# Optimization experiments

Hardware: AMD Instinct MI355X
Metric: run time of the kernel (lower is better)

Reference implementation:

```python
import jax, jax.numpy as jnp
import numpy as np

DIM = 512
DEPTH = 4
HEADS = 8
MLP = 4096
HEAD_DIM = DIM // HEADS
SCALE = HEAD_DIM ** -0.5
EPS = 1e-5


def setup_inputs() -> dict:
    key = jax.random.key(0)
    ks = jax.random.split(key, 14)
    B, C, H, W, D = 1, DIM, 16, 16, 16
    x = jax.random.normal(ks[0], (B, C, H, W, D), dtype=jnp.float32)
    s = 0.02
    inp = {
        'x': x,
        # GroupNorm(1, C) affine params per layer
        'g1': jnp.ones((DEPTH, C), jnp.float32),
        'b1': jnp.zeros((DEPTH, C), jnp.float32),
        'g2': jnp.ones((DEPTH, C), jnp.float32),
        'b2': jnp.zeros((DEPTH, C), jnp.float32),
        # 1x1 conv weights act as channel matmuls
        'wq': jax.random.normal(ks[1], (DEPTH, C, C), jnp.float32) * s,
        'wk': jax.random.normal(ks[2], (DEPTH, C, C), jnp.float32) * s,
        'wv': jax.random.normal(ks[3], (DEPTH, C, C), jnp.float32) * s,
        'wp': jax.random.normal(ks[4], (DEPTH, C, C), jnp.float32) * s,
        'bp': jnp.zeros((DEPTH, C), jnp.float32),
        'w1': jax.random.normal(ks[5], (DEPTH, MLP, C), jnp.float32) * s,
        'bb1': jnp.zeros((DEPTH, MLP), jnp.float32),
        'w2': jax.random.normal(ks[6], (DEPTH, C, MLP), jnp.float32) * s,
        'bb2': jnp.zeros((DEPTH, C), jnp.float32),
    }
    return inp


def _groupnorm1(x, g, b):
    # GroupNorm(num_groups=1): normalize over (C,H,W,D) per sample, per-channel affine
    mu = jnp.mean(x, axis=(1, 2, 3, 4), keepdims=True)
    var = jnp.mean(jnp.square(x - mu), axis=(1, 2, 3, 4), keepdims=True)
    xn = (x - mu) * jax.lax.rsqrt(var + EPS)
    return xn * g[None, :, None, None, None] + b[None, :, None, None, None]


def _attention(x, wq, wk, wv, wp, bp):
    B, C, H, W, D = x.shape
    N = H * W * D
    xf = x.reshape(B, C, N)
    # 1x1 conv == channel matmul; then the module's non-standard view:
    # C split as (head_dim, num_heads)
    q = jnp.einsum('oc,bcn->bon', wq, xf).reshape(B, HEAD_DIM, HEADS, N)
    k = jnp.einsum('oc,bcn->bon', wk, xf).reshape(B, HEAD_DIM, HEADS, N)
    v = jnp.einsum('oc,bcn->bon', wv, xf).reshape(B, HEAD_DIM, HEADS, N)
    attn = jnp.einsum('bchn,bchm->bhnm', q, k) * SCALE  # [B,H,N,N]
    attn = jax.nn.softmax(attn, axis=-1)
    o = jnp.einsum('bhnm,bchm->bchn', attn, v).reshape(B, C, N)
    o = jnp.einsum('oc,bcn->bon', wp, o) + bp[None, :, None]
    return o.reshape(B, C, H, W, D)


def _feedforward(x, w1, bb1, w2, bb2):
    B, C, H, W, D = x.shape
    N = H * W * D
    xf = x.reshape(B, C, N)
    h = jax.nn.relu(jnp.einsum('mc,bcn->bmn', w1, xf) + bb1[None, :, None])
    o = jnp.einsum('cm,bmn->bcn', w2, h) + bb2[None, :, None]
    return o.reshape(B, C, H, W, D)


def reference(x, g1, b1, g2, b2, wq, wk, wv, wp, bp, w1, bb1, w2, bb2):
    for l in range(DEPTH):
        x = x + _attention(_groupnorm1(x, g1[l], b1[l]), wq[l], wk[l], wv[l], wp[l], bp[l])
        x = x + _feedforward(_groupnorm1(x, g2[l], b2[l]), w1[l], bb1[l], w2[l], bb2[l])
    return x
```

## Files before the change

kernel.cpp:

```cpp
#include <hip/hip_runtime.h>

#define CDIM   512
#define NTOK   4096
#define TOT    (CDIM*NTOK)
#define MLPD   4096
#define EPS    1e-5f
#define QSCALE 0.1803368801111204f

typedef _Float16 f16;
typedef _Float16 f16x4 __attribute__((ext_vector_type(4)));
typedef _Float16 f16x8 __attribute__((ext_vector_type(8)));
typedef float    f32x4 __attribute__((ext_vector_type(4)));

typedef __attribute__((address_space(3))) void lds_void;
typedef const __attribute__((address_space(1))) void glb_void;

__device__ __forceinline__ void gload16(const void* g, void* l) {
  __builtin_amdgcn_global_load_lds((glb_void*)g, (lds_void*)l, 16, 0, 0);
}

__device__ __forceinline__ f32x4 zero4() { f32x4 z; z[0]=0.f; z[1]=0.f; z[2]=0.f; z[3]=0.f; return z; }

__global__ __launch_bounds__(256) void cvt_qkv(const float* __restrict__ wq,
                                               const float* __restrict__ wk,
                                               const float* __restrict__ wv,
                                               f16* __restrict__ dst) {
  int i = blockIdx.x * 256 + threadIdx.x;
  int k0 = (i & 63) * 8;
  int rowglob = i >> 6;
  int l = rowglob / 1536;
  int n = rowglob - l * 1536;
  int sect = n >> 9, nn = n & 511;
  int h = nn >> 6, hd = nn & 63;
  int c = hd * 8 + h;
  const float* base = (sect == 0) ? wq : (sect == 1) ? wk : wv;
  const float* src = base + (size_t)l * 262144 + c * 512 + k0;
  float scl = (sect == 0) ? QSCALE : 1.f;
  float4 a = *(const float4*)src;
  float4 b = *(const float4*)(src + 4);
  f16x8 o;
  o[0]=(f16)(a.x*scl); o[1]=(f16)(a.y*scl); o[2]=(f16)(a.z*scl); o[3]=(f16)(a.w*scl);
  o[4]=(f16)(b.x*scl); o[5]=(f16)(b.y*scl); o[6]=(f16)(b.z*scl); o[7]=(f16)(b.w*scl);
  *(f16x8*)&dst[(size_t)l * 786432 + (size_t)n * 512 + k0] = o;
}

__global__ __launch_bounds__(256) void cvt_wp(const float* __restrict__ wp,
                                              f16* __restrict__ dst) {
  int i = blockIdx.x * 256 + threadIdx.x;
  int d0 = (i & 63) * 8;
  int rowglob = i >> 6;
  int l = rowglob >> 9, n = rowglob & 511;
  int h = d0 >> 6;
  const float* src = wp + (size_t)l * 262144 + (size_t)n * 512;
  f16x8 o;
#pragma unroll
  for (int u = 0; u < 8; ++u) {
    int hd = (d0 + u) & 63;
    o[u] = (f16)src[hd * 8 + h];
  }
  *(f16x8*)&dst[(size_t)l * 262144 + (size_t)n * 512 + d0] = o;
}

__global__ __launch_bounds__(256) void cvt_12(const float* __restrict__ w1,
                                              const float* __restrict__ w2,
                                              f16* __restrict__ d1,
                                              f16* __restrict__ d2) {
  int i = blockIdx.x * 256 + threadIdx.x;
  const float* src = blockIdx.y ? w2 : w1;
  f16* dst = blockIdx.y ? d2 : d1;
  size_t e = (size_t)i * 8;
  float4 a = *(const float4*)(src + e);
  float4 b = *(const float4*)(src + e + 4);
  f16x8 o;
  o[0]=(f16)a.x; o[1]=(f16)a.y; o[2]=(f16)a.z; o[3]=(f16)a.w;
  o[4]=(f16)b.x; o[5]=(f16)b.y; o[6]=(f16)b.z; o[7]=(f16)b.w;
  *(f16x8*)&dst[e] = o;
}

template <bool STATS>
__global__ __launch_bounds__(256) void transpose_k(const float* __restrict__ src,
                                                   float* __restrict__ dst,
                                                   int R, int C,
                                                   float* __restrict__ stats) {
  __shared__ float t[64][65];
  int c0 = blockIdx.x * 64, r0 = blockIdx.y * 64;
  float s = 0.f, q = 0.f;
  for (int id = threadIdx.x; id < 1024; id += 256) {
    int row = id >> 4, cc = id & 15;
    float4 v = *(const float4*)&src[(size_t)(r0 + row) * C + c0 + cc * 4];
    *(float4*)&t[row][cc * 4] = v;
    if (STATS) {
      s += (v.x + v.y) + (v.z + v.w);
      q += (v.x*v.x + v.y*v.y) + (v.z*v.z + v.w*v.w);
    }
  }
  __syncthreads();
  for (int id = threadIdx.x; id < 1024; id += 256) {
    int row = id >> 4, cc = id & 15;
    float4 o;
    o.x = t[cc*4+0][row]; o.y = t[cc*4+1][row];
    o.z = t[cc*4+2][row]; o.w = t[cc*4+3][row];
    *(float4*)&dst[(size_t)(c0 + row) * R + r0 + cc * 4] = o;
  }
  if (STATS) {
#pragma unroll
    for (int off = 32; off > 0; off >>= 1) {
      s += __shfl_down(s, off);
      q += __shfl_down(q, off);
    }
    if ((threadIdx.x & 63) == 0) {
      atomicAdd(&stats[0], s);
      atomicAdd(&stats[1], q);
    }
  }
}

__global__ __launch_bounds__(256) void gn_apply2(const float* __restrict__ x,
                                                 const float* __restrict__ stats,
                                                 const float* __restrict__ g,
                                                 const float* __restrict__ b,
                                                 f16* __restrict__ out) {
  int i = blockIdx.x * 256 + threadIdx.x;
  float mu = stats[0] * (1.f / TOT);
  float var = stats[1] * (1.f / TOT) - mu * mu;
  float rs = rsqrtf(var + EPS);
  int c0 = (i & 63) * 8;
  const float4* x4 = (const float4*)x;
  float4 a = x4[i * 2], c = x4[i * 2 + 1];
  float4 G0 = *(const float4*)(g + c0);
  float4 G1 = *(const float4*)(g + c0 + 4);
  float4 B0 = *(const float4*)(b + c0);
  float4 B1 = *(const float4*)(b + c0 + 4);
  f16x8 o;
  o[0]=(f16)((a.x-mu)*rs*G0.x+B0.x); o[1]=(f16)((a.y-mu)*rs*G0.y+B0.y);
  o[2]=(f16)((a.z-mu)*rs*G0.z+B0.z); o[3]=(f16)((a.w-mu)*rs*G0.w+B0.w);
  o[4]=(f16)((c.x-mu)*rs*G1.x+B1.x); o[5]=(f16)((c.y-mu)*rs*G1.y+B1.y);
  o[6]=(f16)((c.z-mu)*rs*G1.z+B1.z); o[7]=(f16)((c.w-mu)*rs*G1.w+B1.w);
  *(f16x8*)&out[(size_t)i * 8] = o;
}

template <int BM, int BN, int MODE>
__global__ __launch_bounds__(256) void hgemm2(const f16* __restrict__ A,
                                              const f16* __restrict__ Bw,
                                              const float* __restrict__ bias,
                                              f16* __restrict__ Cf16,
                                              float* __restrict__ Cf32,
                                              float* __restrict__ stats,
                                              int N, int K) {
  constexpr int MB = BM / 32, NB = BN / 32;
  __shared__ __align__(16) f16 SM[(BM + BN) * 64];
  f16* As = SM;
  f16* Bs = SM + BM * 64;

  const int tid = threadIdx.x;
  const int lane = tid & 63, wid = tid >> 6;
  const int wm = wid >> 1, wn = wid & 1;
  const int m0 = blockIdx.y * BM, n0 = blockIdx.x * BN;
  const int l15 = lane & 15, hi = lane >> 4;

  f32x4 acc[MB][NB];
#pragma unroll
  for (int mb = 0; mb < MB; ++mb)
#pragma unroll
    for (int nb = 0; nb < NB; ++nb) acc[mb][nb] = zero4();

  for (int k0 = 0; k0 < K; k0 += 64) {
#pragma unroll
    for (int j = 0; j < BM / 32; ++j) {
      int flat = j * 256 + tid;
      int row = flat >> 3, c = flat & 7;
      gload16(&A[(size_t)(m0 + row) * K + k0 + ((c ^ (row & 7)) * 8)],
              &As[(j * 256 + wid * 64) * 8]);
    }
#pragma unroll
    for (int j = 0; j < BN / 32; ++j) {
      int flat = j * 256 + tid;
      int row = flat >> 3, c = flat & 7;
      gload16(&Bw[(size_t)(n0 + row) * K + k0 + ((c ^ (row & 7)) * 8)],
              &Bs[(j * 256 + wid * 64) * 8]);
    }
    asm volatile("s_waitcnt vmcnt(0)" ::: "memory");
    __syncthreads();
#pragma unroll
    for (int ks = 0; ks < 2; ++ks) {
      f16x8 af[MB], bf[NB];
#pragma unroll
      for (int mb = 0; mb < MB; ++mb) {
        int row = wm * (BM / 2) + mb * 16 + l15;
        af[mb] = *(const f16x8*)&As[row * 64 + ((ks * 32 + hi * 8) ^ ((row & 7) * 8))];
      }
#pragma unroll
      for (int nb = 0; nb < NB; ++nb) {
        int row = wn * (BN / 2) + nb * 16 + l15;
        bf[nb] = *(const f16x8*)&Bs[row * 64 + ((ks * 32 + hi * 8) ^ ((row & 7) * 8))];
      }
#pragma unroll
      for (int mb = 0; mb < MB; ++mb)
#pragma unroll
        for (int nb = 0; nb < NB; ++nb)
          acc[mb][nb] = __builtin_amdgcn_mfma_f32_16x16x32_f16(af[mb], bf[nb], acc[mb][nb], 0, 0, 0);
    }
    __syncthreads();
  }

  if constexpr (MODE <= 1) {
    f16* Co = SM;
#pragma unroll
    for (int mb = 0; mb < MB; ++mb)
#pragma unroll
      for (int nb = 0; nb < NB; ++nb) {
        int colb = wn * (BN / 2) + nb * 16 + l15;
        float bv = 0.f;
        if constexpr (MODE == 1) bv = bias[n0 + colb];
#pragma unroll
        for (int r = 0; r < 4; ++r) {
          int row = wm * (BM / 2) + mb * 16 + hi * 4 + r;
          float v = acc[mb][nb][r];
          if constexpr (MODE == 1) v = fmaxf(v + bv, 0.f);
          Co[row * BN + (colb ^ ((row & 7) * 8))] = (f16)v;
        }
      }
    __syncthreads();
#pragma unroll
    for (int j = 0; j < BM * BN / 2048; ++j) {
      int flat = j * 256 + tid;
      int row = flat / (BN / 8), c = flat % (BN / 8);
      f16x8 v = *(const f16x8*)&Co[row * BN + ((c * 8) ^ ((row & 7) * 8))];
      *(f16x8*)&Cf16[(size_t)(m0 + row) * N + n0 + c * 8] = v;
    }
  } else {
    float s_acc = 0.f, q_acc = 0.f;
    const int rbase = m0 + wm * (BM / 2) + hi * 4;
#pragma unroll
    for (int mb = 0; mb < MB; ++mb) {
#pragma unroll
      for (int nb = 0; nb < NB; ++nb) {
        int col = n0 + wn * (BN / 2) + nb * 16 + l15;
        float bv = bias[col];
#pragma unroll
        for (int r = 0; r < 4; ++r) {
          int row = rbase + mb * 16 + r;
          float* gp = &Cf32[(size_t)row * N + col];
          float rr = *gp + acc[mb][nb][r] + bv;
          *gp = rr;
          s_acc += rr;
          q_acc += rr * rr;
        }
      }
    }
#pragma unroll
    for (int off = 32; off > 0; off >>= 1) {
      s_acc += __shfl_down(s_acc, off);
      q_acc += __shfl_down(q_acc, off);
    }
    if (lane == 0) {
      atomicAdd(&stats[0], s_acc);
      atomicAdd(&stats[1], q_acc);
    }
  }
}

__global__ __launch_bounds__(256) void perm_v2(const f16* __restrict__ qkv,
                                               f16* __restrict__ vc) {
  __shared__ f16 t[64][72];
  int t0 = blockIdx.x * 64, c0 = blockIdx.y * 64;
  for (int id = threadIdx.x; id < 512; id += 256) {
    int row = id >> 3, cc = id & 7;
    *(f16x8*)&t[row][cc * 8] =
        *(const f16x8*)&qkv[(size_t)(t0 + row) * 1536 + 1024 + c0 + cc * 8];
  }
  __syncthreads();
  for (int id = threadIdx.x; id < 512; id += 256) {
    int row = id >> 3, cc = id & 7;
    f16x8 o;
#pragma unroll
    for (int u = 0; u < 8; ++u) o[u] = t[cc * 8 + u][row];
    *(f16x8*)&vc[(size_t)(c0 + row) * NTOK + t0 + cc * 8] = o;
  }
}

__global__ __launch_bounds__(256) void attn2(const f16* __restrict__ qkv,
                                             const f16* __restrict__ vc,
                                             f16* __restrict__ o) {
  __shared__ __align__(16) f16 Ks[2][64 * 64];
  __shared__ __align__(16) f16 Vs[2][64 * 64];
  __shared__ __align__(16) f16 Ps[64 * 64];

  const int tid = threadIdx.x;
  const int lane = tid & 63, w = tid >> 6;
  const int l15 = lane & 15, hi = lane >> 4;
  const int h = blockIdx.y, q0 = blockIdx.x * 64;

  const f16* qrow = qkv + (size_t)(q0 + w * 16 + l15) * 1536 + h * 64;
  f16x8 qf0 = *(const f16x8*)(qrow + hi * 8);
  f16x8 qf1 = *(const f16x8*)(qrow + 32 + hi * 8);

  float l_run[4] = {0.f, 0.f, 0.f, 0.f};
  f32x4 oacc[4];
#pragma unroll
  for (int nbh = 0; nbh < 4; ++nbh) oacc[nbh] = zero4();

  auto stageK = [&](int buf, int kb) {
#pragma unroll
    for (int j = 0; j < 2; ++j) {
      int flat = j * 256 + tid;
      int rho = flat >> 3, c = flat & 7;
      int key = kb * 64 + ((rho & 15) * 4 + (rho >> 4));
      gload16(qkv + (size_t)key * 1536 + 512 + h * 64 + ((c ^ (rho & 7)) * 8),
              &Ks[buf][(j * 256 + w * 64) * 8]);
    }
  };
  auto stageV = [&](int buf, int kb) {
#pragma unroll
    for (int j = 0; j < 2; ++j) {
      int flat = j * 256 + tid;
      int hd = flat >> 3, c = flat & 7;
      gload16(vc + (size_t)(h * 64 + hd) * NTOK + kb * 64 + ((c ^ (hd & 7)) * 8),
              &Vs[buf][(j * 256 + w * 64) * 8]);
    }
  };

  stageK(0, 0); stageV(0, 0);
  asm volatile("s_waitcnt vmcnt(0)" ::: "memory");
  __syncthreads();

  for (int kb = 0; kb < 64; ++kb) {
    int cur = kb & 1;
    if (kb < 63) { stageK(cur ^ 1, kb + 1); stageV(cur ^ 1, kb + 1); }

    const f16* Kb = &Ks[cur][0];
    f32x4 sacc[4];
#pragma unroll
    for (int nb = 0; nb < 4; ++nb) sacc[nb] = zero4();
    __builtin_amdgcn_s_setprio(1);
#pragma unroll
    for (int nb = 0; nb < 4; ++nb) {
      int row = nb * 16 + l15;
      int sw = (row & 7) * 8;
      f16x8 k0f = *(const f16x8*)&Kb[row * 64 + ((hi * 8) ^ sw)];
      f16x8 k1f = *(const f16x8*)&Kb[row * 64 + ((32 + hi * 8) ^ sw)];
      sacc[nb] = __builtin_amdgcn_mfma_f32_16x16x32_f16(qf0, k0f, sacc[nb], 0, 0, 0);
      sacc[nb] = __builtin_amdgcn_mfma_f32_16x16x32_f16(qf1, k1f, sacc[nb], 0, 0, 0);
    }
    __builtin_amdgcn_s_setprio(0);

#pragma unroll
    for (int r = 0; r < 4; ++r) {
      int prow = w * 16 + hi * 4 + r;
      f16x4 pv;
      float ps = 0.f;
#pragma unroll
      for (int nb = 0; nb < 4; ++nb) {
        float p = exp2f(sacc[nb][r]);
        ps += p;
        pv[nb] = (f16)p;
      }
      *(f16x4*)&Ps[prow * 64 + ((l15 * 4) ^ ((prow & 7) * 8))] = pv;
#pragma unroll
      for (int off = 1; off < 16; off <<= 1) ps += __shfl_xor(ps, off);
      l_run[r] += ps;
    }

    const f16* Vb = &Vs[cur][0];
    {
      int prow = w * 16 + l15;
      int psw = (prow & 7) * 8;
      __builtin_amdgcn_s_setprio(1);
#pragma unroll
      for (int ks2 = 0; ks2 < 2; ++ks2) {
        f16x8 pf = *(const f16x8*)&Ps[prow * 64 + ((ks2 * 32 + hi * 8) ^ psw)];
#pragma unroll
        for (int nbh = 0; nbh < 4; ++nbh) {
          int vrow = nbh * 16 + l15;
          f16x8 vf = *(const f16x8*)&Vb[vrow * 64 + ((ks2 * 32 + hi * 8) ^ ((vrow & 7) * 8))];
          oacc[nbh] = __builtin_amdgcn_mfma_f32_16x16x32_f16(pf, vf, oacc[nbh], 0, 0, 0);
        }
      }
      __builtin_amdgcn_s_setprio(0);
    }
    asm volatile("s_waitcnt vmcnt(0)" ::: "memory");
    __syncthreads();
  }

  float inv[4];
#pragma unroll
  for (int r = 0; r < 4; ++r) inv[r] = 1.f / l_run[r];
  f16* Ot = Ps;
#pragma unroll
  for (int r = 0; r < 4; ++r) {
    int row = w * 16 + hi * 4 + r;
    int sw = (row & 7) * 8;
#pragma unroll
    for (int nbh = 0; nbh < 4; ++nbh) {
      int col = nbh * 16 + l15;
      Ot[row * 64 + (col ^ sw)] = (f16)(oacc[nbh][r] * inv[r]);
    }
  }
  __syncthreads();
#pragma unroll
  for (int j = 0; j < 2; ++j) {
    int flat = j * 256 + tid;
    int row = flat >> 3, c = flat & 7;
    f16x8 v = *(const f16x8*)&Ot[row * 64 + ((c ^ (row & 7)) * 8)];
    *(f16x8*)&o[(size_t)(q0 + row) * 512 + h * 64 + c * 8] = v;
  }
}

extern "C" void kernel_launch(void* const* d_in, const int* in_sizes, int n_in,
                              void* d_out, int out_size, void* d_ws, size_t ws_size,
                              hipStream_t stream) {
  const float* x   = (const float*)d_in[0];
  const float* g1  = (const float*)d_in[1];
  const float* b1  = (const float*)d_in[2];
  const float* g2  = (const float*)d_in[3];
  const float* b2  = (const float*)d_in[4];
  const float* wq  = (const float*)d_in[5];
  const float* wk  = (const float*)d_in[6];
  const float* wv  = (const float*)d_in[7];
  const float* wp  = (const float*)d_in[8];
  const float* bp  = (const float*)d_in[9];
  const float* w1  = (const float*)d_in[10];
  const float* bb1 = (const float*)d_in[11];
  const float* w2  = (const float*)d_in[12];
  const float* bb2 = (const float*)d_in[13];

  char* base = (char*)d_ws;
  size_t off = 0;
  f16* wqkvF = (f16*)(base + off); off += (size_t)4 * 786432 * 2;
  f16* wpF   = (f16*)(base + off); off += (size_t)4 * 262144 * 2;
  f16* w1F   = (f16*)(base + off); off += (size_t)4 * 2097152 * 2;
  f16* w2F   = (f16*)(base + off); off += (size_t)4 * 2097152 * 2;
  float* xcur = (float*)(base + off); off += (size_t)TOT * 4;
  f16* xnT   = (f16*)(base + off); off += (size_t)TOT * 2;
  float* stats_raw = (float*)(base + off); off += 256;
  char* U = base + off; off += 33554432;
  f16* qkvT = (f16*)U;
  f16* vc2  = (f16*)(U + 12582912);
  f16* oatt = (f16*)(U + 16777216);
  f16* hT   = (f16*)U;

  if (ws_size < off) return;

  hipMemsetAsync(stats_raw, 0, 18 * sizeof(float), stream);

  cvt_qkv<<<1536, 256, 0, stream>>>(wq, wk, wv, wqkvF);
  cvt_wp<<<512, 256, 0, stream>>>(wp, wpF);
  cvt_12<<<dim3(4096, 2), 256, 0, stream>>>(w1, w2, w1F, w2F);

  transpose_k<true><<<dim3(64, 8), 256, 0, stream>>>(x, xcur, 512, 4096, stats_raw);

  for (int l = 0; l < 4; ++l) {
    gn_apply2<<<1024, 256, 0, stream>>>(xcur, stats_raw + 2 * (2 * l),
                                        g1 + l * CDIM, b1 + l * CDIM, xnT);
    hgemm2<128, 128, 0><<<dim3(12, 32), 256, 0, stream>>>(
        xnT, wqkvF + (size_t)l * 786432, nullptr, qkvT, nullptr, nullptr, 1536, 512);
    perm_v2<<<dim3(64, 8), 256, 0, stream>>>(qkvT, vc2);
    attn2<<<dim3(64, 8), 256, 0, stream>>>(qkvT, vc2, oatt);
    hgemm2<64, 128, 2><<<dim3(4, 64), 256, 0, stream>>>(
        oatt, wpF + (size_t)l * 262144, bp + l * CDIM, nullptr, xcur,
        stats_raw + 2 * (2 * l + 1), 512, 512);

    gn_apply2<<<1024, 256, 0, stream>>>(xcur, stats_raw + 2 * (2 * l + 1),
                                        g2 + l * CDIM, b2 + l * CDIM, xnT);
    hgemm2<128, 128, 1><<<dim3(32, 32), 256, 0, stream>>>(
        xnT, w1F + (size_t)l * 2097152, bb1 + l * MLPD, hT, nullptr, nullptr, 4096, 512);
    hgemm2<64, 128, 2><<<dim3(4, 64), 256, 0, stream>>>(
        hT, w2F + (size_t)l * 2097152, bb2 + l * CDIM, nullptr, xcur,
        stats_raw + 2 * (2 * l + 2), 512, 4096);
  }

  transpose_k<false><<<dim3(8, 64), 256, 0, stream>>>(xcur, (float*)d_out, 4096, 512, nullptr);
}
```

Measured before the change: 1.294 ms.

## Fuse GroupNorm into GEMM A-loads and split attention over keys

The separate GroupNorm-apply kernels are removed. The QKV and FFN1 GEMMs now read the fp32 activations directly, normalise them with the precomputed stats and affine parameters, and store fp16 tiles into shared memory. This saves two launches per layer and the write and re-read of the normalised buffer, but the A-tile load becomes a synchronous register path and reads twice as many bytes. Attention is split into two halves over the key range, which doubles the block count to fill the device better. A new combine kernel sums the unnormalised partial outputs and row sums, at the cost of extra fp16 partial traffic and one more launch.

```diff
diff --git a/kernel.cpp b/kernel.cpp
--- a/kernel.cpp
+++ b/kernel.cpp
@@ -115,33 +115,13 @@
   }
 }
 
-__global__ __launch_bounds__(256) void gn_apply2(const float* __restrict__ x,
-                                                 const float* __restrict__ stats,
-                                                 const float* __restrict__ g,
-                                                 const float* __restrict__ b,
-                                                 f16* __restrict__ out) {
-  int i = blockIdx.x * 256 + threadIdx.x;
-  float mu = stats[0] * (1.f / TOT);
-  float var = stats[1] * (1.f / TOT) - mu * mu;
-  float rs = rsqrtf(var + EPS);
-  int c0 = (i & 63) * 8;
-  const float4* x4 = (const float4*)x;
-  float4 a = x4[i * 2], c = x4[i * 2 + 1];
-  float4 G0 = *(const float4*)(g + c0);
-  float4 G1 = *(const float4*)(g + c0 + 4);
-  float4 B0 = *(const float4*)(b + c0);
-  float4 B1 = *(const float4*)(b + c0 + 4);
-  f16x8 o;
-  o[0]=(f16)((a.x-mu)*rs*G0.x+B0.x); o[1]=(f16)((a.y-mu)*rs*G0.y+B0.y);
-  o[2]=(f16)((a.z-mu)*rs*G0.z+B0.z); o[3]=(f16)((a.w-mu)*rs*G0.w+B0.w);
-  o[4]=(f16)((c.x-mu)*rs*G1.x+B1.x); o[5]=(f16)((c.y-mu)*rs*G1.y+B1.y);
-  o[6]=(f16)((c.z-mu)*rs*G1.z+B1.z); o[7]=(f16)((c.w-mu)*rs*G1.w+B1.w);
-  *(f16x8*)&out[(size_t)i * 8] = o;
-}
-
-template <int BM, int BN, int MODE>
+template <int BM, int BN, int MODE, bool FUSE>
 __global__ __launch_bounds__(256) void hgemm2(const f16* __restrict__ A,
+                                              const float* __restrict__ Af32,
                                               const f16* __restrict__ Bw,
+                                              const float* __restrict__ gnst,
+                                              const float* __restrict__ g,
+                                              const float* __restrict__ b,
                                               const float* __restrict__ bias,
                                               f16* __restrict__ Cf16,
                                               float* __restrict__ Cf32,
@@ -158,6 +138,13 @@
   const int m0 = blockIdx.y * BM, n0 = blockIdx.x * BN;
   const int l15 = lane & 15, hi = lane >> 4;
 
+  float mu = 0.f, rs = 0.f;
+  if constexpr (FUSE) {
+    mu = gnst[0] * (1.f / TOT);
+    float var = gnst[1] * (1.f / TOT) - mu * mu;
+    rs = rsqrtf(var + EPS);
+  }
+
   f32x4 acc[MB][NB];
 #pragma unroll
   for (int mb = 0; mb < MB; ++mb)
@@ -165,12 +152,35 @@
     for (int nb = 0; nb < NB; ++nb) acc[mb][nb] = zero4();
 
   for (int k0 = 0; k0 < K; k0 += 64) {
-#pragma unroll
-    for (int j = 0; j < BM / 32; ++j) {
-      int flat = j * 256 + tid;
-      int row = flat >> 3, c = flat & 7;
-      gload16(&A[(size_t)(m0 + row) * K + k0 + ((c ^ (row & 7)) * 8)],
-              &As[(j * 256 + wid * 64) * 8]);
+    if constexpr (FUSE) {
+      int ch = k0 + (tid & 7) * 8;
+      float4 G0 = *(const float4*)&g[ch], G1 = *(const float4*)&g[ch + 4];
+      float4 B0 = *(const float4*)&b[ch], B1 = *(const float4*)&b[ch + 4];
+      float gg[8] = {G0.x*rs, G0.y*rs, G0.z*rs, G0.w*rs, G1.x*rs, G1.y*rs, G1.z*rs, G1.w*rs};
+      float bb[8] = {B0.x - mu*gg[0], B0.y - mu*gg[1], B0.z - mu*gg[2], B0.w - mu*gg[3],
+                     B1.x - mu*gg[4], B1.y - mu*gg[5], B1.z - mu*gg[6], B1.w - mu*gg[7]};
+#pragma unroll
+      for (int j = 0; j < BM / 32; ++j) {
+        int flat = j * 256 + tid;
+        int row = flat >> 3, c8 = flat & 7;
+        const float* srcp = &Af32[(size_t)(m0 + row) * K + ch];
+        float4 a0 = *(const float4*)srcp;
+        float4 a1 = *(const float4*)(srcp + 4);
+        f16x8 ov;
+        ov[0]=(f16)(a0.x*gg[0]+bb[0]); ov[1]=(f16)(a0.y*gg[1]+bb[1]);
+        ov[2]=(f16)(a0.z*gg[2]+bb[2]); ov[3]=(f16)(a0.w*gg[3]+bb[3]);
+        ov[4]=(f16)(a1.x*gg[4]+bb[4]); ov[5]=(f16)(a1.y*gg[5]+bb[5]);
+        ov[6]=(f16)(a1.z*gg[6]+bb[6]); ov[7]=(f16)(a1.w*gg[7]+bb[7]);
+        *(f16x8*)&As[row * 64 + ((c8 ^ (row & 7)) * 8)] = ov;
+      }
+    } else {
+#pragma unroll
+      for (int j = 0; j < BM / 32; ++j) {
+        int flat = j * 256 + tid;
+        int row = flat >> 3, c = flat & 7;
+        gload16(&A[(size_t)(m0 + row) * K + k0 + ((c ^ (row & 7)) * 8)],
+                &As[(j * 256 + wid * 64) * 8]);
+      }
     }
 #pragma unroll
     for (int j = 0; j < BN / 32; ++j) {
@@ -281,7 +291,8 @@
 
 __global__ __launch_bounds__(256) void attn2(const f16* __restrict__ qkv,
                                              const f16* __restrict__ vc,
-                                             f16* __restrict__ o) {
+                                             f16* __restrict__ Op,
+                                             float* __restrict__ lp) {
   __shared__ __align__(16) f16 Ks[2][64 * 64];
   __shared__ __align__(16) f16 Vs[2][64 * 64];
   __shared__ __align__(16) f16 Ps[64 * 64];
@@ -289,7 +300,9 @@
   const int tid = threadIdx.x;
   const int lane = tid & 63, w = tid >> 6;
   const int l15 = lane & 15, hi = lane >> 4;
-  const int h = blockIdx.y, q0 = blockIdx.x * 64;
+  const int id = blockIdx.x;
+  const int h = id & 7, split = (id >> 3) & 1, q0 = (id >> 4) * 64;
+  const int kbase = split * 32;
 
   const f16* qrow = qkv + (size_t)(q0 + w * 16 + l15) * 1536 + h * 64;
   f16x8 qf0 = *(const f16x8*)(qrow + hi * 8);
@@ -320,13 +333,13 @@
     }
   };
 
-  stageK(0, 0); stageV(0, 0);
+  stageK(0, kbase); stageV(0, kbase);
   asm volatile("s_waitcnt vmcnt(0)" ::: "memory");
   __syncthreads();
 
-  for (int kb = 0; kb < 64; ++kb) {
-    int cur = kb & 1;
-    if (kb < 63) { stageK(cur ^ 1, kb + 1); stageV(cur ^ 1, kb + 1); }
+  for (int kb2 = 0; kb2 < 32; ++kb2) {
+    int cur = kb2 & 1;
+    if (kb2 < 31) { stageK(cur ^ 1, kbase + kb2 + 1); stageV(cur ^ 1, kbase + kb2 + 1); }
 
     const f16* Kb = &Ks[cur][0];
     f32x4 sacc[4];
@@ -382,9 +395,11 @@
     __syncthreads();
   }
 
-  float inv[4];
-#pragma unroll
-  for (int r = 0; r < 4; ++r) inv[r] = 1.f / l_run[r];
+  if (l15 == 0) {
+#pragma unroll
+    for (int r = 0; r < 4; ++r)
+      lp[(size_t)(split * 8 + h) * NTOK + q0 + w * 16 + hi * 4 + r] = l_run[r];
+  }
   f16* Ot = Ps;
 #pragma unroll
   for (int r = 0; r < 4; ++r) {
@@ -393,7 +408,7 @@
 #pragma unroll
     for (int nbh = 0; nbh < 4; ++nbh) {
       int col = nbh * 16 + l15;
-      Ot[row * 64 + (col ^ sw)] = (f16)(oacc[nbh][r] * inv[r]);
+      Ot[row * 64 + (col ^ sw)] = (f16)oacc[nbh][r];
     }
   }
   __syncthreads();
@@ -402,8 +417,25 @@
     int flat = j * 256 + tid;
     int row = flat >> 3, c = flat & 7;
     f16x8 v = *(const f16x8*)&Ot[row * 64 + ((c ^ (row & 7)) * 8)];
-    *(f16x8*)&o[(size_t)(q0 + row) * 512 + h * 64 + c * 8] = v;
-  }
+    *(f16x8*)&Op[(size_t)split * TOT + (size_t)(q0 + row) * 512 + h * 64 + c * 8] = v;
+  }
+}
+
+__global__ __launch_bounds__(256) void attn_combine(const f16* __restrict__ Op,
+                                                    const float* __restrict__ lp,
+                                                    f16* __restrict__ oatt) {
+  int i = blockIdx.x * 256 + threadIdx.x;
+  int tok = i >> 6;
+  int c0 = (i & 63) * 8;
+  int h = c0 >> 6;
+  f16x8 a = *(const f16x8*)&Op[(size_t)tok * 512 + c0];
+  f16x8 b = *(const f16x8*)&Op[(size_t)TOT + (size_t)tok * 512 + c0];
+  float l = lp[(size_t)h * NTOK + tok] + lp[(size_t)(8 + h) * NTOK + tok];
+  float inv = 1.f / l;
+  f16x8 o;
+#pragma unroll
+  for (int u = 0; u < 8; ++u) o[u] = (f16)(((float)a[u] + (float)b[u]) * inv);
+  *(f16x8*)&oatt[(size_t)tok * 512 + c0] = o;
 }
 
 extern "C" void kernel_launch(void* const* d_in, const int* in_sizes, int n_in,
@@ -431,12 +463,13 @@
   f16* w1F   = (f16*)(base + off); off += (size_t)4 * 2097152 * 2;
   f16* w2F   = (f16*)(base + off); off += (size_t)4 * 2097152 * 2;
   float* xcur = (float*)(base + off); off += (size_t)TOT * 4;
-  f16* xnT   = (f16*)(base + off); off += (size_t)TOT * 2;
   float* stats_raw = (float*)(base + off); off += 256;
+  float* lp = (float*)(base + off); off += (size_t)2 * 8 * NTOK * 4;
   char* U = base + off; off += 33554432;
   f16* qkvT = (f16*)U;
   f16* vc2  = (f16*)(U + 12582912);
-  f16* oatt = (f16*)(U + 16777216);
+  f16* Op   = (f16*)(U + 16777216);
+  f16* oatt = (f16*)(U + 25165824);
   f16* hT   = (f16*)U;
 
   if (ws_size < off) return;
@@ -450,23 +483,22 @@
   transpose_k<true><<<dim3(64, 8), 256, 0, stream>>>(x, xcur, 512, 4096, stats_raw);
 
   for (int l = 0; l < 4; ++l) {
-    gn_apply2<<<1024, 256, 0, stream>>>(xcur, stats_raw + 2 * (2 * l),
-                                        g1 + l * CDIM, b1 + l * CDIM, xnT);
-    hgemm2<128, 128, 0><<<dim3(12, 32), 256, 0, stream>>>(
-        xnT, wqkvF + (size_t)l * 786432, nullptr, qkvT, nullptr, nullptr, 1536, 512);
+    hgemm2<128, 128, 0, true><<<dim3(12, 32), 256, 0, stream>>>(
+        nullptr, xcur, wqkvF + (size_t)l * 786432, stats_raw + 2 * (2 * l),
+        g1 + l * CDIM, b1 + l * CDIM, nullptr, qkvT, nullptr, nullptr, 1536, 512);
     perm_v2<<<dim3(64, 8), 256, 0, stream>>>(qkvT, vc2);
-    attn2<<<dim3(64, 8), 256, 0, stream>>>(qkvT, vc2, oatt);
-    hgemm2<64, 128, 2><<<dim3(4, 64), 256, 0, stream>>>(
-        oatt, wpF + (size_t)l * 262144, bp + l * CDIM, nullptr, xcur,
-        stats_raw + 2 * (2 * l + 1), 512, 512);
-
-    gn_apply2<<<1024, 256, 0, stream>>>(xcur, stats_raw + 2 * (2 * l + 1),
-                                        g2 + l * CDIM, b2 + l * CDIM, xnT);
-    hgemm2<128, 128, 1><<<dim3(32, 32), 256, 0, stream>>>(
-        xnT, w1F + (size_t)l * 2097152, bb1 + l * MLPD, hT, nullptr, nullptr, 4096, 512);
-    hgemm2<64, 128, 2><<<dim3(4, 64), 256, 0, stream>>>(
-        hT, w2F + (size_t)l * 2097152, bb2 + l * CDIM, nullptr, xcur,
-        stats_raw + 2 * (2 * l + 2), 512, 4096);
+    attn2<<<1024, 256, 0, stream>>>(qkvT, vc2, Op, lp);
+    attn_combine<<<1024, 256, 0, stream>>>(Op, lp, oatt);
+    hgemm2<64, 128, 2, false><<<dim3(4, 64), 256, 0, stream>>>(
+        oatt, nullptr, wpF + (size_t)l * 262144, nullptr, nullptr, nullptr,
+        bp + l * CDIM, nullptr, xcur, stats_raw + 2 * (2 * l + 1), 512, 512);
+
+    hgemm2<128, 128, 1, true><<<dim3(32, 32), 256, 0, stream>>>(
+        nullptr, xcur, w1F + (size_t)l * 2097152, stats_raw + 2 * (2 * l + 1),
+        g2 + l * CDIM, b2 + l * CDIM, bb1 + l * MLPD, hT, nullptr, nullptr, 4096, 512);
+    hgemm2<64, 128, 2, false><<<dim3(4, 64), 256, 0, stream>>>(
+        hT, nullptr, w2F + (size_t)l * 2097152, nullptr, nullptr, nullptr,
+        bb2 + l * CDIM, nullptr, xcur, stats_raw + 2 * (2 * l + 2), 512, 4096);
   }
 
   transpose_k<false><<<dim3(8, 64), 256, 0, stream>>>(xcur, (float*)d_out, 4096, 512, nullptr);
```

Measured after the change: 1.296 ms. About the same (+0.2%).
